# Optimization experiments

Measured on AMD Instinct MI355X. Metric: run time of the kernel, lower is better.

Reference implementation:

```python
import jax, jax.numpy as jnp
import numpy as np

N_NODES = 50000
N_GENES = 256
N_EDGES = 800000
NUM_ITERATIONS = 10  # init_kwargs: num_iterations
SPARSITY = 0.3       # fraction of nonzero entries in expression matrix


def setup_inputs() -> dict:
    key = jax.random.key(0)
    k1, k2, k3, k4 = jax.random.split(key, 4)
    vals = jax.random.uniform(k1, (N_NODES, N_GENES), dtype=jnp.float32)
    keep = jax.random.uniform(k2, (N_NODES, N_GENES)) < SPARSITY
    x = jnp.where(keep, vals, 0.0)
    edge_index = jax.random.randint(k3, (2, N_EDGES), 0, N_NODES, dtype=jnp.int64)
    edge_weight = jax.random.uniform(k4, (N_EDGES,), dtype=jnp.float32)
    return {"x": x, "edge_index": edge_index, "edge_weight": edge_weight}


def reference(x, edge_index, edge_weight):
    # FeaturePropagation with mask=True, max_imputation_per_cell=None,
    # early_stopping=False: iterate x <- A @ x, then clamp known (nonzero)
    # entries back to their original values.
    n = x.shape[0]
    dst = edge_index[0]  # sparse COO row indices
    src = edge_index[1]  # sparse COO col indices
    orig = x
    known = x != 0

    def step(h, _):
        # SpMM: out[dst] += w * h[src]   (torch.sparse.mm(adj, x))
        msgs = edge_weight[:, None] * h[src]              # [E, G]
        h = jax.ops.segment_sum(msgs, dst, num_segments=n)  # [N, G]
        h = jnp.where(known, orig, h)  # reset known entries
        return h, None

    out, _ = jax.lax.scan(step, x, None, length=NUM_ITERATIONS)
    return out
```

## Files before the change

kernel.cpp:

```cpp
#include <hip/hip_runtime.h>

#define N_NODES 50000
#define N_GENES 256
#define N_EDGES 800000
#define NUM_ITERS 10
#define SCAN_BLK 1024
#define N_SCAN_BLKS ((N_NODES + SCAN_BLK - 1) / SCAN_BLK)

typedef unsigned short u16;

struct u16x4 { u16 x, y, z, w; };

static __device__ __forceinline__ float bf2f(u16 b) {
    return __uint_as_float(((unsigned)b) << 16);
}
static __device__ __forceinline__ u16 f2bf(float f) {
    unsigned u = __float_as_uint(f);
    return (u16)((u + 0x7fffu + ((u >> 16) & 1u)) >> 16);
}


__global__ void hist_kernel(const int* __restrict__ dst, int* __restrict__ counts) {
    int e = blockIdx.x * blockDim.x + threadIdx.x;
    if (e < N_EDGES) atomicAdd(&counts[dst[e]], 1);
}

__global__ __launch_bounds__(SCAN_BLK) void scan1_kernel(
        const int* __restrict__ counts, int* __restrict__ offs,
        int* __restrict__ bsums) {
    int i = blockIdx.x * SCAN_BLK + threadIdx.x;
    int lane = threadIdx.x & 63, wid = threadIdx.x >> 6;
    int v = (i < N_NODES) ? counts[i] : 0;
    int x = v;
    #pragma unroll
    for (int o = 1; o < 64; o <<= 1) {
        int t = __shfl_up(x, o, 64);
        if (lane >= o) x += t;
    }
    __shared__ int wsum[16];
    if (lane == 63) wsum[wid] = x;
    __syncthreads();
    if (wid == 0 && lane < 16) {
        int y = wsum[lane];
        #pragma unroll
        for (int o = 1; o < 16; o <<= 1) {
            int t = __shfl_up(y, o, 64);
            if (lane >= o) y += t;
        }
        wsum[lane] = y;
    }
    __syncthreads();
    int pref = (wid > 0) ? wsum[wid - 1] : 0;
    int incl = x + pref;
    if (i < N_NODES) offs[i] = incl - v;
    if (threadIdx.x == SCAN_BLK - 1) bsums[blockIdx.x] = incl;
}

__global__ void scan2_kernel(const int* __restrict__ bsums,
                             int* __restrict__ bpref,
                             int* __restrict__ offs_total) {
    int lane = threadIdx.x;
    int v = (lane < N_SCAN_BLKS) ? bsums[lane] : 0;
    int x = v;
    #pragma unroll
    for (int o = 1; o < 64; o <<= 1) {
        int t = __shfl_up(x, o, 64);
        if (lane >= o) x += t;
    }
    if (lane < N_SCAN_BLKS) bpref[lane] = x - v;
    if (lane == 63) offs_total[0] = x;
}

__global__ __launch_bounds__(SCAN_BLK) void scan3_kernel(
        int* __restrict__ offs, const int* __restrict__ bpref,
        int* __restrict__ cursor) {
    int i = blockIdx.x * SCAN_BLK + threadIdx.x;
    if (i < N_NODES) {
        int o = offs[i] + bpref[blockIdx.x];
        offs[i] = o;
        cursor[i] = o;
    }
}

__global__ void scatter_kernel(const int* __restrict__ dst,
                               const int* __restrict__ src,
                               const float* __restrict__ w,
                               int* __restrict__ cursor,
                               int2* __restrict__ edges) {
    int e = blockIdx.x * blockDim.x + threadIdx.x;
    if (e < N_EDGES) {
        int d = dst[e];
        int p = atomicAdd(&cursor[d], 1);
        edges[p] = make_int2(src[e], __float_as_int(w[e]));
    }
}

__global__ __launch_bounds__(256) void cvt_kernel(const float* __restrict__ x,
                                                  u16* __restrict__ xb) {
    int i = (blockIdx.x * blockDim.x + threadIdx.x) * 8;
    if (i >= N_NODES * N_GENES) return;
    float4 a = *reinterpret_cast<const float4*>(&x[i]);
    float4 b = *reinterpret_cast<const float4*>(&x[i + 4]);
    u16x4 r0 = { f2bf(a.x), f2bf(a.y), f2bf(a.z), f2bf(a.w) };
    u16x4 r1 = { f2bf(b.x), f2bf(b.y), f2bf(b.z), f2bf(b.w) };
    *reinterpret_cast<u16x4*>(&xb[i])     = r0;
    *reinterpret_cast<u16x4*>(&xb[i + 4]) = r1;
}


__global__ __launch_bounds__(256) void prop_kernel_b(
        const u16* __restrict__ hin,
        const u16* __restrict__ xb,
        const int* __restrict__ offsets,
        const int2* __restrict__ edges,
        u16* __restrict__ out) {
    int node = blockIdx.x * 4 + (threadIdx.x >> 6);
    if (node >= N_NODES) return;
    int lane = threadIdx.x & 63;
    int g4 = lane << 2;

    int beg = offsets[node];
    int end = offsets[node + 1];

    float a0 = 0.f, a1 = 0.f, a2 = 0.f, a3 = 0.f;

    for (int base = beg; base < end; base += 64) {
        int cnt = end - base;
        if (cnt > 64) cnt = 64;
        int2 el = make_int2(0, 0);
        if (lane < cnt) el = edges[base + lane];

        int k = 0;
        for (; k + 8 <= cnt; k += 8) {
            int s[8]; float w[8];
            #pragma unroll
            for (int j = 0; j < 8; ++j) {
                s[j] = __shfl(el.x, k + j);
                w[j] = __int_as_float(__shfl(el.y, k + j));
            }
            u16x4 r[8];
            #pragma unroll
            for (int j = 0; j < 8; ++j)
                r[j] = *reinterpret_cast<const u16x4*>(&hin[(size_t)s[j] * N_GENES + g4]);
            #pragma unroll
            for (int j = 0; j < 8; ++j) {
                a0 += w[j] * bf2f(r[j].x);
                a1 += w[j] * bf2f(r[j].y);
                a2 += w[j] * bf2f(r[j].z);
                a3 += w[j] * bf2f(r[j].w);
            }
        }
        for (; k < cnt; ++k) {
            int   s = __shfl(el.x, k);
            float w = __int_as_float(__shfl(el.y, k));
            u16x4 r = *reinterpret_cast<const u16x4*>(&hin[(size_t)s * N_GENES + g4]);
            a0 += w * bf2f(r.x);
            a1 += w * bf2f(r.y);
            a2 += w * bf2f(r.z);
            a3 += w * bf2f(r.w);
        }
    }

    size_t idx = (size_t)node * N_GENES + g4;
    u16x4 o = *reinterpret_cast<const u16x4*>(&xb[idx]);
    u16x4 res;
    res.x = o.x ? o.x : f2bf(a0);
    res.y = o.y ? o.y : f2bf(a1);
    res.z = o.z ? o.z : f2bf(a2);
    res.w = o.w ? o.w : f2bf(a3);
    *reinterpret_cast<u16x4*>(&out[idx]) = res;
}

__global__ __launch_bounds__(256) void prop_kernel_final(
        const u16* __restrict__ hin,
        const float* __restrict__ x,
        const int* __restrict__ offsets,
        const int2* __restrict__ edges,
        float* __restrict__ out) {
    int node = blockIdx.x * 4 + (threadIdx.x >> 6);
    if (node >= N_NODES) return;
    int lane = threadIdx.x & 63;
    int g4 = lane << 2;

    int beg = offsets[node];
    int end = offsets[node + 1];

    float a0 = 0.f, a1 = 0.f, a2 = 0.f, a3 = 0.f;

    for (int base = beg; base < end; base += 64) {
        int cnt = end - base;
        if (cnt > 64) cnt = 64;
        int2 el = make_int2(0, 0);
        if (lane < cnt) el = edges[base + lane];

        int k = 0;
        for (; k + 8 <= cnt; k += 8) {
            int s[8]; float w[8];
            #pragma unroll
            for (int j = 0; j < 8; ++j) {
                s[j] = __shfl(el.x, k + j);
                w[j] = __int_as_float(__shfl(el.y, k + j));
            }
            u16x4 r[8];
            #pragma unroll
            for (int j = 0; j < 8; ++j)
                r[j] = *reinterpret_cast<const u16x4*>(&hin[(size_t)s[j] * N_GENES + g4]);
            #pragma unroll
            for (int j = 0; j < 8; ++j) {
                a0 += w[j] * bf2f(r[j].x);
                a1 += w[j] * bf2f(r[j].y);
                a2 += w[j] * bf2f(r[j].z);
                a3 += w[j] * bf2f(r[j].w);
            }
        }
        for (; k < cnt; ++k) {
            int   s = __shfl(el.x, k);
            float w = __int_as_float(__shfl(el.y, k));
            u16x4 r = *reinterpret_cast<const u16x4*>(&hin[(size_t)s * N_GENES + g4]);
            a0 += w * bf2f(r.x);
            a1 += w * bf2f(r.y);
            a2 += w * bf2f(r.z);
            a3 += w * bf2f(r.w);
        }
    }

    size_t idx = (size_t)node * N_GENES + g4;
    float4 o = *reinterpret_cast<const float4*>(&x[idx]);
    float4 res;
    res.x = (o.x != 0.f) ? o.x : a0;
    res.y = (o.y != 0.f) ? o.y : a1;
    res.z = (o.z != 0.f) ? o.z : a2;
    res.w = (o.w != 0.f) ? o.w : a3;
    *reinterpret_cast<float4*>(&out[idx]) = res;
}


static inline size_t align_up(size_t x, size_t a) { return (x + a - 1) & ~(a - 1); }

extern "C" void kernel_launch(void* const* d_in, const int* in_sizes, int n_in,
                              void* d_out, int out_size, void* d_ws, size_t ws_size,
                              hipStream_t stream) {
    const float* x    = (const float*)d_in[0];
    const int*   eidx = (const int*)d_in[1];
    const float* ew   = (const float*)d_in[2];
    float*       out  = (float*)d_out;

    const int* dst = eidx;
    const int* src = eidx + N_EDGES;

    char* ws = (char*)d_ws;
    size_t off = 0;
    u16*   xb      = (u16*) (ws + off); off += align_up((size_t)N_NODES * N_GENES * 2, 256);
    u16*   hb0     = (u16*) (ws + off); off += align_up((size_t)N_NODES * N_GENES * 2, 256);
    int2*  edges   = (int2*)(ws + off); off += align_up((size_t)N_EDGES * 8, 256);
    int*   counts  = (int*) (ws + off); off += align_up((size_t)N_NODES * 4, 256);
    int*   offsets = (int*) (ws + off); off += align_up((size_t)(N_NODES + 1) * 4, 256);
    int*   cursor  = (int*) (ws + off); off += align_up((size_t)N_NODES * 4, 256);
    int*   bsums   = (int*) (ws + off); off += align_up((size_t)N_SCAN_BLKS * 4, 256);
    int*   bpref   = (int*) (ws + off); off += align_up((size_t)N_SCAN_BLKS * 4, 256);
    (void)ws_size;

    u16* hbO = (u16*)d_out;

    hipMemsetAsync(counts, 0, (size_t)N_NODES * 4, stream);
    hist_kernel<<<(N_EDGES + 255) / 256, 256, 0, stream>>>(dst, counts);
    scan1_kernel<<<N_SCAN_BLKS, SCAN_BLK, 0, stream>>>(counts, offsets, bsums);
    scan2_kernel<<<1, 64, 0, stream>>>(bsums, bpref, &offsets[N_NODES]);
    scan3_kernel<<<N_SCAN_BLKS, SCAN_BLK, 0, stream>>>(offsets, bpref, cursor);
    scatter_kernel<<<(N_EDGES + 255) / 256, 256, 0, stream>>>(dst, src, ew, cursor, edges);
    cvt_kernel<<<(N_NODES * N_GENES / 8 + 255) / 256, 256, 0, stream>>>(x, xb);

    const int grid = (N_NODES + 3) / 4;
    const u16* hin = xb;
    for (int it = 0; it < NUM_ITERS - 1; ++it) {
        u16* hout = (it & 1) ? hbO : hb0;
        prop_kernel_b<<<grid, 256, 0, stream>>>(hin, xb, offsets, edges, hout);
        hin = hout;
    }
    prop_kernel_final<<<grid, 256, 0, stream>>>(hin, x, offsets, edges, out);
}
```

Baseline: 768.7 us.

## Slice gene dimension into 32-wide planes for cache-resident gather propagation

Splits the bf16 feature matrix into 8 gene slices of 32 columns, each stored as a contiguous [N,32] plane. Each block handles one slice, so the gathered working set per slice is about 3.2MB and can stay in L2/MALL. Four edges are processed in parallel per wave with a cross-lane reduction. Source indices are packed as u16, which holds only because N_NODES fits in 16 bits, and weights go into a separate array. The cost is that the CSR edge list is re-read once per slice, and there are more shuffles plus a reduction per node.

```diff
diff --git a/kernel.cpp b/kernel.cpp
--- a/kernel.cpp
+++ b/kernel.cpp
@@ -7,8 +7,14 @@
 #define SCAN_BLK 1024
 #define N_SCAN_BLKS ((N_NODES + SCAN_BLK - 1) / SCAN_BLK)
 
+#define SLICE_G 32
+#define N_SLICES 8
+#define NODES_PER_WAVE 8
+#define NODES_PER_BLOCK 32
+#define BLKS_PER_SLICE ((N_NODES + NODES_PER_BLOCK - 1) / NODES_PER_BLOCK)
+#define PROP_GRID (BLKS_PER_SLICE * N_SLICES)
+
 typedef unsigned short u16;
-
 struct u16x4 { u16 x, y, z, w; };
 
 static __device__ __forceinline__ float bf2f(u16 b) {
@@ -86,152 +92,176 @@
                                const int* __restrict__ src,
                                const float* __restrict__ w,
                                int* __restrict__ cursor,
-                               int2* __restrict__ edges) {
+                               u16* __restrict__ ssrc,
+                               float* __restrict__ sw) {
     int e = blockIdx.x * blockDim.x + threadIdx.x;
     if (e < N_EDGES) {
         int d = dst[e];
         int p = atomicAdd(&cursor[d], 1);
-        edges[p] = make_int2(src[e], __float_as_int(w[e]));
-    }
-}
-
-__global__ __launch_bounds__(256) void cvt_kernel(const float* __restrict__ x,
-                                                  u16* __restrict__ xb) {
-    int i = (blockIdx.x * blockDim.x + threadIdx.x) * 8;
-    if (i >= N_NODES * N_GENES) return;
-    float4 a = *reinterpret_cast<const float4*>(&x[i]);
-    float4 b = *reinterpret_cast<const float4*>(&x[i + 4]);
+        ssrc[p] = (u16)src[e];
+        sw[p]   = w[e];
+    }
+}
+
+__global__ __launch_bounds__(256) void cvt_slice_kernel(const float* __restrict__ x,
+                                                        u16* __restrict__ xs) {
+    int base = (blockIdx.x * blockDim.x + threadIdx.x) * 8;
+    if (base >= N_NODES * N_GENES) return;
+    int node = base >> 8;
+    int gene = base & 255;
+    int slice = gene >> 5;
+    int g = gene & 31;
+    float4 a = *reinterpret_cast<const float4*>(&x[base]);
+    float4 b = *reinterpret_cast<const float4*>(&x[base + 4]);
     u16x4 r0 = { f2bf(a.x), f2bf(a.y), f2bf(a.z), f2bf(a.w) };
     u16x4 r1 = { f2bf(b.x), f2bf(b.y), f2bf(b.z), f2bf(b.w) };
-    *reinterpret_cast<u16x4*>(&xb[i])     = r0;
-    *reinterpret_cast<u16x4*>(&xb[i + 4]) = r1;
-}
-
-
-__global__ __launch_bounds__(256) void prop_kernel_b(
+    size_t o = (size_t)slice * N_NODES * SLICE_G + (size_t)node * SLICE_G + g;
+    *reinterpret_cast<u16x4*>(&xs[o])     = r0;
+    *reinterpret_cast<u16x4*>(&xs[o + 4]) = r1;
+}
+
+
+__global__ __launch_bounds__(256) void prop_s_b(
         const u16* __restrict__ hin,
-        const u16* __restrict__ xb,
+        const u16* __restrict__ xs,
         const int* __restrict__ offsets,
-        const int2* __restrict__ edges,
+        const u16* __restrict__ ssrc,
+        const float* __restrict__ sw,
         u16* __restrict__ out) {
-    int node = blockIdx.x * 4 + (threadIdx.x >> 6);
-    if (node >= N_NODES) return;
-    int lane = threadIdx.x & 63;
-    int g4 = lane << 2;
-
-    int beg = offsets[node];
-    int end = offsets[node + 1];
-
-    float a0 = 0.f, a1 = 0.f, a2 = 0.f, a3 = 0.f;
-
-    for (int base = beg; base < end; base += 64) {
-        int cnt = end - base;
-        if (cnt > 64) cnt = 64;
-        int2 el = make_int2(0, 0);
-        if (lane < cnt) el = edges[base + lane];
-
-        int k = 0;
-        for (; k + 8 <= cnt; k += 8) {
-            int s[8]; float w[8];
-            #pragma unroll
-            for (int j = 0; j < 8; ++j) {
-                s[j] = __shfl(el.x, k + j);
-                w[j] = __int_as_float(__shfl(el.y, k + j));
-            }
-            u16x4 r[8];
-            #pragma unroll
-            for (int j = 0; j < 8; ++j)
-                r[j] = *reinterpret_cast<const u16x4*>(&hin[(size_t)s[j] * N_GENES + g4]);
-            #pragma unroll
-            for (int j = 0; j < 8; ++j) {
-                a0 += w[j] * bf2f(r[j].x);
-                a1 += w[j] * bf2f(r[j].y);
-                a2 += w[j] * bf2f(r[j].z);
-                a3 += w[j] * bf2f(r[j].w);
-            }
-        }
-        for (; k < cnt; ++k) {
-            int   s = __shfl(el.x, k);
-            float w = __int_as_float(__shfl(el.y, k));
-            u16x4 r = *reinterpret_cast<const u16x4*>(&hin[(size_t)s * N_GENES + g4]);
-            a0 += w * bf2f(r.x);
-            a1 += w * bf2f(r.y);
-            a2 += w * bf2f(r.z);
-            a3 += w * bf2f(r.w);
-        }
-    }
-
-    size_t idx = (size_t)node * N_GENES + g4;
-    u16x4 o = *reinterpret_cast<const u16x4*>(&xb[idx]);
-    u16x4 res;
-    res.x = o.x ? o.x : f2bf(a0);
-    res.y = o.y ? o.y : f2bf(a1);
-    res.z = o.z ? o.z : f2bf(a2);
-    res.w = o.w ? o.w : f2bf(a3);
-    *reinterpret_cast<u16x4*>(&out[idx]) = res;
-}
-
-__global__ __launch_bounds__(256) void prop_kernel_final(
+    int slice = blockIdx.x & 7;
+    int blk   = blockIdx.x >> 3;
+    int wid = threadIdx.x >> 6, lane = threadIdx.x & 63;
+    int slot = lane >> 4;
+    int g2   = (lane & 15) << 1;
+    const u16* hs = hin + (size_t)slice * N_NODES * SLICE_G;
+
+    int node_base = blk * NODES_PER_BLOCK + wid * NODES_PER_WAVE;
+    for (int n = 0; n < NODES_PER_WAVE; ++n) {
+        int node = node_base + n;
+        if (node >= N_NODES) break;
+        int beg = offsets[node], end = offsets[node + 1];
+        float ax = 0.f, ay = 0.f;
+
+        for (int base = beg; base < end; base += 64) {
+            int cnt = end - base;
+            if (cnt > 64) cnt = 64;
+            int sv = 0; float wv = 0.f;
+            if (lane < cnt) {
+                sv = __builtin_nontemporal_load(&ssrc[base + lane]);
+                wv = __builtin_nontemporal_load(&sw[base + lane]);
+            }
+            int kmax = (cnt + 3) >> 2;
+            int k = 0;
+            for (; k + 4 <= kmax; k += 4) {
+                int e0 = (k + 0) * 4 + slot, e1 = (k + 1) * 4 + slot;
+                int e2 = (k + 2) * 4 + slot, e3 = (k + 3) * 4 + slot;
+                int   s0 = __shfl(sv, e0), s1 = __shfl(sv, e1);
+                int   s2 = __shfl(sv, e2), s3 = __shfl(sv, e3);
+                float w0 = __shfl(wv, e0), w1 = __shfl(wv, e1);
+                float w2 = __shfl(wv, e2), w3 = __shfl(wv, e3);
+                unsigned p0 = *reinterpret_cast<const unsigned*>(&hs[s0 * SLICE_G + g2]);
+                unsigned p1 = *reinterpret_cast<const unsigned*>(&hs[s1 * SLICE_G + g2]);
+                unsigned p2 = *reinterpret_cast<const unsigned*>(&hs[s2 * SLICE_G + g2]);
+                unsigned p3 = *reinterpret_cast<const unsigned*>(&hs[s3 * SLICE_G + g2]);
+                ax += w0 * bf2f((u16)p0) + w1 * bf2f((u16)p1)
+                    + w2 * bf2f((u16)p2) + w3 * bf2f((u16)p3);
+                ay += w0 * bf2f((u16)(p0 >> 16)) + w1 * bf2f((u16)(p1 >> 16))
+                    + w2 * bf2f((u16)(p2 >> 16)) + w3 * bf2f((u16)(p3 >> 16));
+            }
+            for (; k < kmax; ++k) {
+                int e = k * 4 + slot;
+                int   s = __shfl(sv, e);
+                float w = __shfl(wv, e);
+                unsigned p = *reinterpret_cast<const unsigned*>(&hs[s * SLICE_G + g2]);
+                ax += w * bf2f((u16)p);
+                ay += w * bf2f((u16)(p >> 16));
+            }
+        }
+
+        ax += __shfl_xor(ax, 16); ax += __shfl_xor(ax, 32);
+        ay += __shfl_xor(ay, 16); ay += __shfl_xor(ay, 32);
+
+        if (slot == 0) {
+            size_t o = (size_t)slice * N_NODES * SLICE_G + (size_t)node * SLICE_G + g2;
+            unsigned ox = __builtin_nontemporal_load(reinterpret_cast<const unsigned*>(&xs[o]));
+            u16 b0 = (u16)(ox & 0xFFFFu), b1 = (u16)(ox >> 16);
+            u16 r0 = b0 ? b0 : f2bf(ax);
+            u16 r1 = b1 ? b1 : f2bf(ay);
+            unsigned res = (unsigned)r0 | ((unsigned)r1 << 16);
+            __builtin_nontemporal_store(res, reinterpret_cast<unsigned*>(&out[o]));
+        }
+    }
+}
+
+__global__ __launch_bounds__(256) void prop_s_final(
         const u16* __restrict__ hin,
         const float* __restrict__ x,
         const int* __restrict__ offsets,
-        const int2* __restrict__ edges,
+        const u16* __restrict__ ssrc,
+        const float* __restrict__ sw,
         float* __restrict__ out) {
-    int node = blockIdx.x * 4 + (threadIdx.x >> 6);
-    if (node >= N_NODES) return;
-    int lane = threadIdx.x & 63;
-    int g4 = lane << 2;
-
-    int beg = offsets[node];
-    int end = offsets[node + 1];
-
-    float a0 = 0.f, a1 = 0.f, a2 = 0.f, a3 = 0.f;
-
-    for (int base = beg; base < end; base += 64) {
-        int cnt = end - base;
-        if (cnt > 64) cnt = 64;
-        int2 el = make_int2(0, 0);
-        if (lane < cnt) el = edges[base + lane];
-
-        int k = 0;
-        for (; k + 8 <= cnt; k += 8) {
-            int s[8]; float w[8];
-            #pragma unroll
-            for (int j = 0; j < 8; ++j) {
-                s[j] = __shfl(el.x, k + j);
-                w[j] = __int_as_float(__shfl(el.y, k + j));
-            }
-            u16x4 r[8];
-            #pragma unroll
-            for (int j = 0; j < 8; ++j)
-                r[j] = *reinterpret_cast<const u16x4*>(&hin[(size_t)s[j] * N_GENES + g4]);
-            #pragma unroll
-            for (int j = 0; j < 8; ++j) {
-                a0 += w[j] * bf2f(r[j].x);
-                a1 += w[j] * bf2f(r[j].y);
-                a2 += w[j] * bf2f(r[j].z);
-                a3 += w[j] * bf2f(r[j].w);
-            }
-        }
-        for (; k < cnt; ++k) {
-            int   s = __shfl(el.x, k);
-            float w = __int_as_float(__shfl(el.y, k));
-            u16x4 r = *reinterpret_cast<const u16x4*>(&hin[(size_t)s * N_GENES + g4]);
-            a0 += w * bf2f(r.x);
-            a1 += w * bf2f(r.y);
-            a2 += w * bf2f(r.z);
-            a3 += w * bf2f(r.w);
-        }
-    }
-
-    size_t idx = (size_t)node * N_GENES + g4;
-    float4 o = *reinterpret_cast<const float4*>(&x[idx]);
-    float4 res;
-    res.x = (o.x != 0.f) ? o.x : a0;
-    res.y = (o.y != 0.f) ? o.y : a1;
-    res.z = (o.z != 0.f) ? o.z : a2;
-    res.w = (o.w != 0.f) ? o.w : a3;
-    *reinterpret_cast<float4*>(&out[idx]) = res;
+    int slice = blockIdx.x & 7;
+    int blk   = blockIdx.x >> 3;
+    int wid = threadIdx.x >> 6, lane = threadIdx.x & 63;
+    int slot = lane >> 4;
+    int g2   = (lane & 15) << 1;
+    const u16* hs = hin + (size_t)slice * N_NODES * SLICE_G;
+
+    int node_base = blk * NODES_PER_BLOCK + wid * NODES_PER_WAVE;
+    for (int n = 0; n < NODES_PER_WAVE; ++n) {
+        int node = node_base + n;
+        if (node >= N_NODES) break;
+        int beg = offsets[node], end = offsets[node + 1];
+        float ax = 0.f, ay = 0.f;
+
+        for (int base = beg; base < end; base += 64) {
+            int cnt = end - base;
+            if (cnt > 64) cnt = 64;
+            int sv = 0; float wv = 0.f;
+            if (lane < cnt) {
+                sv = __builtin_nontemporal_load(&ssrc[base + lane]);
+                wv = __builtin_nontemporal_load(&sw[base + lane]);
+            }
+            int kmax = (cnt + 3) >> 2;
+            int k = 0;
+            for (; k + 4 <= kmax; k += 4) {
+                int e0 = (k + 0) * 4 + slot, e1 = (k + 1) * 4 + slot;
+                int e2 = (k + 2) * 4 + slot, e3 = (k + 3) * 4 + slot;
+                int   s0 = __shfl(sv, e0), s1 = __shfl(sv, e1);
+                int   s2 = __shfl(sv, e2), s3 = __shfl(sv, e3);
+                float w0 = __shfl(wv, e0), w1 = __shfl(wv, e1);
+                float w2 = __shfl(wv, e2), w3 = __shfl(wv, e3);
+                unsigned p0 = *reinterpret_cast<const unsigned*>(&hs[s0 * SLICE_G + g2]);
+                unsigned p1 = *reinterpret_cast<const unsigned*>(&hs[s1 * SLICE_G + g2]);
+                unsigned p2 = *reinterpret_cast<const unsigned*>(&hs[s2 * SLICE_G + g2]);
+                unsigned p3 = *reinterpret_cast<const unsigned*>(&hs[s3 * SLICE_G + g2]);
+                ax += w0 * bf2f((u16)p0) + w1 * bf2f((u16)p1)
+                    + w2 * bf2f((u16)p2) + w3 * bf2f((u16)p3);
+                ay += w0 * bf2f((u16)(p0 >> 16)) + w1 * bf2f((u16)(p1 >> 16))
+                    + w2 * bf2f((u16)(p2 >> 16)) + w3 * bf2f((u16)(p3 >> 16));
+            }
+            for (; k < kmax; ++k) {
+                int e = k * 4 + slot;
+                int   s = __shfl(sv, e);
+                float w = __shfl(wv, e);
+                unsigned p = *reinterpret_cast<const unsigned*>(&hs[s * SLICE_G + g2]);
+                ax += w * bf2f((u16)p);
+                ay += w * bf2f((u16)(p >> 16));
+            }
+        }
+
+        ax += __shfl_xor(ax, 16); ax += __shfl_xor(ax, 32);
+        ay += __shfl_xor(ay, 16); ay += __shfl_xor(ay, 32);
+
+        if (slot == 0) {
+            size_t xo = (size_t)node * N_GENES + slice * SLICE_G + g2;
+            float2 o = *reinterpret_cast<const float2*>(&x[xo]);
+            float2 r;
+            r.x = (o.x != 0.f) ? o.x : ax;
+            r.y = (o.y != 0.f) ? o.y : ay;
+            *reinterpret_cast<float2*>(&out[xo]) = r;
+        }
+    }
 }
 
 
@@ -250,9 +280,10 @@
 
     char* ws = (char*)d_ws;
     size_t off = 0;
-    u16*   xb      = (u16*) (ws + off); off += align_up((size_t)N_NODES * N_GENES * 2, 256);
-    u16*   hb0     = (u16*) (ws + off); off += align_up((size_t)N_NODES * N_GENES * 2, 256);
-    int2*  edges   = (int2*)(ws + off); off += align_up((size_t)N_EDGES * 8, 256);
+    u16*   xs      = (u16*) (ws + off); off += align_up((size_t)N_NODES * N_GENES * 2, 256);
+    u16*   hsA     = (u16*) (ws + off); off += align_up((size_t)N_NODES * N_GENES * 2, 256);
+    u16*   ssrc    = (u16*) (ws + off); off += align_up((size_t)N_EDGES * 2, 256);
+    float* swt     = (float*)(ws + off); off += align_up((size_t)N_EDGES * 4, 256);
     int*   counts  = (int*) (ws + off); off += align_up((size_t)N_NODES * 4, 256);
     int*   offsets = (int*) (ws + off); off += align_up((size_t)(N_NODES + 1) * 4, 256);
     int*   cursor  = (int*) (ws + off); off += align_up((size_t)N_NODES * 4, 256);
@@ -260,22 +291,21 @@
     int*   bpref   = (int*) (ws + off); off += align_up((size_t)N_SCAN_BLKS * 4, 256);
     (void)ws_size;
 
-    u16* hbO = (u16*)d_out;
+    u16* hsB = (u16*)d_out;
 
     hipMemsetAsync(counts, 0, (size_t)N_NODES * 4, stream);
     hist_kernel<<<(N_EDGES + 255) / 256, 256, 0, stream>>>(dst, counts);
     scan1_kernel<<<N_SCAN_BLKS, SCAN_BLK, 0, stream>>>(counts, offsets, bsums);
     scan2_kernel<<<1, 64, 0, stream>>>(bsums, bpref, &offsets[N_NODES]);
     scan3_kernel<<<N_SCAN_BLKS, SCAN_BLK, 0, stream>>>(offsets, bpref, cursor);
-    scatter_kernel<<<(N_EDGES + 255) / 256, 256, 0, stream>>>(dst, src, ew, cursor, edges);
-    cvt_kernel<<<(N_NODES * N_GENES / 8 + 255) / 256, 256, 0, stream>>>(x, xb);
-
-    const int grid = (N_NODES + 3) / 4;
-    const u16* hin = xb;
+    scatter_kernel<<<(N_EDGES + 255) / 256, 256, 0, stream>>>(dst, src, ew, cursor, ssrc, swt);
+    cvt_slice_kernel<<<(N_NODES * N_GENES / 8 + 255) / 256, 256, 0, stream>>>(x, xs);
+
+    const u16* hin = xs;
     for (int it = 0; it < NUM_ITERS - 1; ++it) {
-        u16* hout = (it & 1) ? hbO : hb0;
-        prop_kernel_b<<<grid, 256, 0, stream>>>(hin, xb, offsets, edges, hout);
+        u16* hout = (it & 1) ? hsB : hsA;
+        prop_s_b<<<PROP_GRID, 256, 0, stream>>>(hin, xs, offsets, ssrc, swt, hout);
         hin = hout;
     }
-    prop_kernel_final<<<grid, 256, 0, stream>>>(hin, x, offsets, edges, out);
-}
+    prop_s_final<<<PROP_GRID, 256, 0, stream>>>(hin, x, offsets, ssrc, swt, out);
+}
```

After: 1.798 ms. +133.8%, slower.

## Split feature matrix into two 128-gene slices to shrink gather working set

Applied to the files above, without the earlier changes.

The bf16 feature matrix is stored as two contiguous 128-gene slices, and each propagation block handles one slice for four nodes, with blocks interleaved so both slices of a node group are processed close together. Each slice is 12.8 MB instead of one 25.6 MB matrix, meant to improve cache hit rates for the random neighbour gathers. Edge and known-value reads and bf16 stores use nontemporal hints so they are less likely to evict gathered rows. In exchange, edge lists and offsets are read twice (once per slice), and each lane does narrower 4-byte loads.

```diff
diff --git a/kernel.cpp b/kernel.cpp
--- a/kernel.cpp
+++ b/kernel.cpp
@@ -7,8 +7,11 @@
 #define SCAN_BLK 1024
 #define N_SCAN_BLKS ((N_NODES + SCAN_BLK - 1) / SCAN_BLK)
 
+#define SLICE_G 128
+#define N_SLICES 2
+#define PROP_GRID 25000
+
 typedef unsigned short u16;
-
 struct u16x4 { u16 x, y, z, w; };
 
 static __device__ __forceinline__ float bf2f(u16 b) {
@@ -95,143 +98,147 @@
     }
 }
 
-__global__ __launch_bounds__(256) void cvt_kernel(const float* __restrict__ x,
-                                                  u16* __restrict__ xb) {
-    int i = (blockIdx.x * blockDim.x + threadIdx.x) * 8;
-    if (i >= N_NODES * N_GENES) return;
-    float4 a = *reinterpret_cast<const float4*>(&x[i]);
-    float4 b = *reinterpret_cast<const float4*>(&x[i + 4]);
+__global__ __launch_bounds__(256) void cvt_slice_kernel(const float* __restrict__ x,
+                                                        u16* __restrict__ xs) {
+    int base = (blockIdx.x * blockDim.x + threadIdx.x) * 8;
+    if (base >= N_NODES * N_GENES) return;
+    int node = base >> 8;
+    int gene = base & 255;
+    int slice = gene >> 7;
+    int g = gene & 127;
+    float4 a = *reinterpret_cast<const float4*>(&x[base]);
+    float4 b = *reinterpret_cast<const float4*>(&x[base + 4]);
     u16x4 r0 = { f2bf(a.x), f2bf(a.y), f2bf(a.z), f2bf(a.w) };
     u16x4 r1 = { f2bf(b.x), f2bf(b.y), f2bf(b.z), f2bf(b.w) };
-    *reinterpret_cast<u16x4*>(&xb[i])     = r0;
-    *reinterpret_cast<u16x4*>(&xb[i + 4]) = r1;
-}
-
-
-__global__ __launch_bounds__(256) void prop_kernel_b(
+    size_t o = (size_t)slice * (N_NODES * SLICE_G) + (size_t)node * SLICE_G + g;
+    *reinterpret_cast<u16x4*>(&xs[o])     = r0;
+    *reinterpret_cast<u16x4*>(&xs[o + 4]) = r1;
+}
+
+
+__global__ __launch_bounds__(256) void prop2_b(
         const u16* __restrict__ hin,
-        const u16* __restrict__ xb,
+        const u16* __restrict__ xs,
         const int* __restrict__ offsets,
         const int2* __restrict__ edges,
         u16* __restrict__ out) {
-    int node = blockIdx.x * 4 + (threadIdx.x >> 6);
-    if (node >= N_NODES) return;
+    int b = blockIdx.x;
+    int slice = ((b & 7) < 4) ? 0 : 1;
+    int idx = (b >> 3) * 4 + (b & 3);
+    int node = idx * 4 + (threadIdx.x >> 6);
     int lane = threadIdx.x & 63;
-    int g4 = lane << 2;
-
-    int beg = offsets[node];
-    int end = offsets[node + 1];
-
-    float a0 = 0.f, a1 = 0.f, a2 = 0.f, a3 = 0.f;
+    int g2 = lane << 1;
+
+    const u16* hs = hin + (size_t)slice * (N_NODES * SLICE_G);
+    int beg = offsets[node], end = offsets[node + 1];
+    float ax = 0.f, ay = 0.f;
 
     for (int base = beg; base < end; base += 64) {
         int cnt = end - base;
         if (cnt > 64) cnt = 64;
         int2 el = make_int2(0, 0);
-        if (lane < cnt) el = edges[base + lane];
+        if (lane < cnt) {
+            long long ev = __builtin_nontemporal_load(
+                reinterpret_cast<const long long*>(&edges[base + lane]));
+            el.x = (int)ev;
+            el.y = (int)(ev >> 32);
+        }
 
         int k = 0;
         for (; k + 8 <= cnt; k += 8) {
-            int s[8]; float w[8];
+            int s[8]; float w[8]; unsigned p[8];
             #pragma unroll
             for (int j = 0; j < 8; ++j) {
                 s[j] = __shfl(el.x, k + j);
                 w[j] = __int_as_float(__shfl(el.y, k + j));
             }
-            u16x4 r[8];
             #pragma unroll
             for (int j = 0; j < 8; ++j)
-                r[j] = *reinterpret_cast<const u16x4*>(&hin[(size_t)s[j] * N_GENES + g4]);
-            #pragma unroll
-            for (int j = 0; j < 8; ++j) {
-                a0 += w[j] * bf2f(r[j].x);
-                a1 += w[j] * bf2f(r[j].y);
-                a2 += w[j] * bf2f(r[j].z);
-                a3 += w[j] * bf2f(r[j].w);
+                p[j] = *reinterpret_cast<const unsigned*>(&hs[(size_t)s[j] * SLICE_G + g2]);
+            #pragma unroll
+            for (int j = 0; j < 8; ++j) {
+                ax += w[j] * bf2f((u16)p[j]);
+                ay += w[j] * bf2f((u16)(p[j] >> 16));
             }
         }
         for (; k < cnt; ++k) {
             int   s = __shfl(el.x, k);
             float w = __int_as_float(__shfl(el.y, k));
-            u16x4 r = *reinterpret_cast<const u16x4*>(&hin[(size_t)s * N_GENES + g4]);
-            a0 += w * bf2f(r.x);
-            a1 += w * bf2f(r.y);
-            a2 += w * bf2f(r.z);
-            a3 += w * bf2f(r.w);
-        }
-    }
-
-    size_t idx = (size_t)node * N_GENES + g4;
-    u16x4 o = *reinterpret_cast<const u16x4*>(&xb[idx]);
-    u16x4 res;
-    res.x = o.x ? o.x : f2bf(a0);
-    res.y = o.y ? o.y : f2bf(a1);
-    res.z = o.z ? o.z : f2bf(a2);
-    res.w = o.w ? o.w : f2bf(a3);
-    *reinterpret_cast<u16x4*>(&out[idx]) = res;
-}
-
-__global__ __launch_bounds__(256) void prop_kernel_final(
+            unsigned p = *reinterpret_cast<const unsigned*>(&hs[(size_t)s * SLICE_G + g2]);
+            ax += w * bf2f((u16)p);
+            ay += w * bf2f((u16)(p >> 16));
+        }
+    }
+
+    size_t o = (size_t)slice * (N_NODES * SLICE_G) + (size_t)node * SLICE_G + g2;
+    unsigned ox = __builtin_nontemporal_load(reinterpret_cast<const unsigned*>(&xs[o]));
+    u16 b0 = (u16)(ox & 0xFFFFu), b1 = (u16)(ox >> 16);
+    u16 r0 = b0 ? b0 : f2bf(ax);
+    u16 r1 = b1 ? b1 : f2bf(ay);
+    unsigned res = (unsigned)r0 | ((unsigned)r1 << 16);
+    __builtin_nontemporal_store(res, reinterpret_cast<unsigned*>(&out[o]));
+}
+
+__global__ __launch_bounds__(256) void prop2_final(
         const u16* __restrict__ hin,
         const float* __restrict__ x,
         const int* __restrict__ offsets,
         const int2* __restrict__ edges,
         float* __restrict__ out) {
-    int node = blockIdx.x * 4 + (threadIdx.x >> 6);
-    if (node >= N_NODES) return;
+    int b = blockIdx.x;
+    int slice = ((b & 7) < 4) ? 0 : 1;
+    int idx = (b >> 3) * 4 + (b & 3);
+    int node = idx * 4 + (threadIdx.x >> 6);
     int lane = threadIdx.x & 63;
-    int g4 = lane << 2;
-
-    int beg = offsets[node];
-    int end = offsets[node + 1];
-
-    float a0 = 0.f, a1 = 0.f, a2 = 0.f, a3 = 0.f;
+    int g2 = lane << 1;
+
+    const u16* hs = hin + (size_t)slice * (N_NODES * SLICE_G);
+    int beg = offsets[node], end = offsets[node + 1];
+    float ax = 0.f, ay = 0.f;
 
     for (int base = beg; base < end; base += 64) {
         int cnt = end - base;
         if (cnt > 64) cnt = 64;
         int2 el = make_int2(0, 0);
-        if (lane < cnt) el = edges[base + lane];
+        if (lane < cnt) {
+            long long ev = __builtin_nontemporal_load(
+                reinterpret_cast<const long long*>(&edges[base + lane]));
+            el.x = (int)ev;
+            el.y = (int)(ev >> 32);
+        }
 
         int k = 0;
         for (; k + 8 <= cnt; k += 8) {
-            int s[8]; float w[8];
+            int s[8]; float w[8]; unsigned p[8];
             #pragma unroll
             for (int j = 0; j < 8; ++j) {
                 s[j] = __shfl(el.x, k + j);
                 w[j] = __int_as_float(__shfl(el.y, k + j));
             }
-            u16x4 r[8];
             #pragma unroll
             for (int j = 0; j < 8; ++j)
-                r[j] = *reinterpret_cast<const u16x4*>(&hin[(size_t)s[j] * N_GENES + g4]);
-            #pragma unroll
-            for (int j = 0; j < 8; ++j) {
-                a0 += w[j] * bf2f(r[j].x);
-                a1 += w[j] * bf2f(r[j].y);
-                a2 += w[j] * bf2f(r[j].z);
-                a3 += w[j] * bf2f(r[j].w);
+                p[j] = *reinterpret_cast<const unsigned*>(&hs[(size_t)s[j] * SLICE_G + g2]);
+            #pragma unroll
+            for (int j = 0; j < 8; ++j) {
+                ax += w[j] * bf2f((u16)p[j]);
+                ay += w[j] * bf2f((u16)(p[j] >> 16));
             }
         }
         for (; k < cnt; ++k) {
             int   s = __shfl(el.x, k);
             float w = __int_as_float(__shfl(el.y, k));
-            u16x4 r = *reinterpret_cast<const u16x4*>(&hin[(size_t)s * N_GENES + g4]);
-            a0 += w * bf2f(r.x);
-            a1 += w * bf2f(r.y);
-            a2 += w * bf2f(r.z);
-            a3 += w * bf2f(r.w);
-        }
-    }
-
-    size_t idx = (size_t)node * N_GENES + g4;
-    float4 o = *reinterpret_cast<const float4*>(&x[idx]);
-    float4 res;
-    res.x = (o.x != 0.f) ? o.x : a0;
-    res.y = (o.y != 0.f) ? o.y : a1;
-    res.z = (o.z != 0.f) ? o.z : a2;
-    res.w = (o.w != 0.f) ? o.w : a3;
-    *reinterpret_cast<float4*>(&out[idx]) = res;
+            unsigned p = *reinterpret_cast<const unsigned*>(&hs[(size_t)s * SLICE_G + g2]);
+            ax += w * bf2f((u16)p);
+            ay += w * bf2f((u16)(p >> 16));
+        }
+    }
+
+    size_t xo = (size_t)node * N_GENES + slice * SLICE_G + g2;
+    float2 o = *reinterpret_cast<const float2*>(&x[xo]);
+    float2 r;
+    r.x = (o.x != 0.f) ? o.x : ax;
+    r.y = (o.y != 0.f) ? o.y : ay;
+    *reinterpret_cast<float2*>(&out[xo]) = r;
 }
 
 
@@ -250,8 +257,8 @@
 
     char* ws = (char*)d_ws;
     size_t off = 0;
-    u16*   xb      = (u16*) (ws + off); off += align_up((size_t)N_NODES * N_GENES * 2, 256);
-    u16*   hb0     = (u16*) (ws + off); off += align_up((size_t)N_NODES * N_GENES * 2, 256);
+    u16*   xs      = (u16*) (ws + off); off += align_up((size_t)N_NODES * N_GENES * 2, 256);
+    u16*   hsA     = (u16*) (ws + off); off += align_up((size_t)N_NODES * N_GENES * 2, 256);
     int2*  edges   = (int2*)(ws + off); off += align_up((size_t)N_EDGES * 8, 256);
     int*   counts  = (int*) (ws + off); off += align_up((size_t)N_NODES * 4, 256);
     int*   offsets = (int*) (ws + off); off += align_up((size_t)(N_NODES + 1) * 4, 256);
@@ -260,7 +267,7 @@
     int*   bpref   = (int*) (ws + off); off += align_up((size_t)N_SCAN_BLKS * 4, 256);
     (void)ws_size;
 
-    u16* hbO = (u16*)d_out;
+    u16* hsB = (u16*)d_out;
 
     hipMemsetAsync(counts, 0, (size_t)N_NODES * 4, stream);
     hist_kernel<<<(N_EDGES + 255) / 256, 256, 0, stream>>>(dst, counts);
@@ -268,14 +275,13 @@
     scan2_kernel<<<1, 64, 0, stream>>>(bsums, bpref, &offsets[N_NODES]);
     scan3_kernel<<<N_SCAN_BLKS, SCAN_BLK, 0, stream>>>(offsets, bpref, cursor);
     scatter_kernel<<<(N_EDGES + 255) / 256, 256, 0, stream>>>(dst, src, ew, cursor, edges);
-    cvt_kernel<<<(N_NODES * N_GENES / 8 + 255) / 256, 256, 0, stream>>>(x, xb);
-
-    const int grid = (N_NODES + 3) / 4;
-    const u16* hin = xb;
+    cvt_slice_kernel<<<(N_NODES * N_GENES / 8 + 255) / 256, 256, 0, stream>>>(x, xs);
+
+    const u16* hin = xs;
     for (int it = 0; it < NUM_ITERS - 1; ++it) {
-        u16* hout = (it & 1) ? hbO : hb0;
-        prop_kernel_b<<<grid, 256, 0, stream>>>(hin, xb, offsets, edges, hout);
+        u16* hout = (it & 1) ? hsB : hsA;
+        prop2_b<<<PROP_GRID, 256, 0, stream>>>(hin, xs, offsets, edges, hout);
         hin = hout;
     }
-    prop_kernel_final<<<grid, 256, 0, stream>>>(hin, x, offsets, edges, out);
-}
+    prop2_final<<<PROP_GRID, 256, 0, stream>>>(hin, x, offsets, edges, out);
+}
```

Result: slower. 881.8 us (+14.7%).
